# Kernel optimization log

Hardware: AMD Instinct MI355X
Metric: run time of the kernel (lower is better)

The kernel has to match this reference:

```python
import jax, jax.numpy as jnp
import numpy as np

ALPHA = 0.3        # Keras LeakyReLU default negative_slope
NUM_STEPS = 16     # fixed-step Dormand-Prince (see notes)
DEPTH = 10
HID = 1024
LOOK = 30
BATCH = 16384


def _leaky(x):
    return jnp.where(x > 0, x, ALPHA * x)


def _mlp(y, W1, b1, W2, b2, W3, b3):
    # drift f(y): 30 -> 1024 -> 1024 -> 30, autonomous (t unused)
    h = _leaky(jnp.dot(y, W1) + b1)
    h = _leaky(jnp.dot(h, W2) + b2)
    return jnp.dot(h, W3) + b3


def _dopri5_step(y, h, params):
    f = lambda z: _mlp(z, *params)
    k1 = f(y)
    k2 = f(y + h * (1.0 / 5.0) * k1)
    k3 = f(y + h * (3.0 / 40.0 * k1 + 9.0 / 40.0 * k2))
    k4 = f(y + h * (44.0 / 45.0 * k1 - 56.0 / 15.0 * k2 + 32.0 / 9.0 * k3))
    k5 = f(y + h * (19372.0 / 6561.0 * k1 - 25360.0 / 2187.0 * k2
                    + 64448.0 / 6561.0 * k3 - 212.0 / 729.0 * k4))
    k6 = f(y + h * (9017.0 / 3168.0 * k1 - 355.0 / 33.0 * k2
                    + 46732.0 / 5247.0 * k3 + 49.0 / 176.0 * k4
                    - 5103.0 / 18656.0 * k5))
    # 5th-order solution (b row of the Dormand-Prince tableau)
    return y + h * (35.0 / 384.0 * k1 + 500.0 / 1113.0 * k3
                    + 125.0 / 192.0 * k4 - 2187.0 / 6784.0 * k5
                    + 11.0 / 84.0 * k6)


def _solve_block(y0, params):
    # integrate dy/dt = f(y) from t=0 to t=1 with fixed step h
    h = 1.0 / NUM_STEPS
    def step(y, _):
        return _dopri5_step(y, h, params), None
    y, _ = jax.lax.scan(step, y0, None, length=NUM_STEPS)
    return y


def setup_inputs() -> dict:
    key = jax.random.key(0)
    ks = jax.random.split(key, 9)
    y0 = jax.random.normal(ks[0], (BATCH, 1, LOOK), dtype=jnp.float32)
    s1 = 1.0 / np.sqrt(LOOK)
    s2 = 1.0 / np.sqrt(HID)
    W1 = jax.random.normal(ks[1], (DEPTH, LOOK, HID), dtype=jnp.float32) * s1
    b1 = jnp.zeros((DEPTH, HID), dtype=jnp.float32)
    W2 = jax.random.normal(ks[2], (DEPTH, HID, HID), dtype=jnp.float32) * s2
    b2 = jnp.zeros((DEPTH, HID), dtype=jnp.float32)
    W3 = jax.random.normal(ks[3], (DEPTH, HID, LOOK), dtype=jnp.float32) * s2
    b3 = jnp.zeros((DEPTH, LOOK), dtype=jnp.float32)
    Wf = jax.random.normal(ks[4], (LOOK, 1), dtype=jnp.float32) * s1
    bf = jnp.zeros((1,), dtype=jnp.float32)
    return {"y0": y0, "W1": W1, "b1": b1, "W2": W2, "b2": b2,
            "W3": W3, "b3": b3, "Wf": Wf, "bf": bf}


def reference(y0, W1, b1, W2, b2, W3, b3, Wf, bf):
    # sequentially apply DEPTH ODE blocks, each with its own drift MLP
    def block(y, p):
        return _solve_block(y, p), None
    y, _ = jax.lax.scan(block, y0, (W1, b1, W2, b2, W3, b3))
    # final readout Dense(output_dim=1)
    return jnp.dot(y, Wf) + bf  # (B, 1, 1)
```

## Files before the change

### kernel.cpp

```cpp
#include <hip/hip_runtime.h>

#define BATCH 16384
#define LOOK 30
#define HID 1024
#define DEPTH 10
#define NSTEPS 16
#define ALPHA 0.3f

typedef short bf16x8 __attribute__((ext_vector_type(8)));
typedef float f32x4 __attribute__((ext_vector_type(4)));

__device__ __forceinline__ float leaky(float x) { return x > 0.f ? x : ALPHA * x; }

__device__ __forceinline__ unsigned short f2bf(float x) {
  unsigned u = __builtin_bit_cast(unsigned, x);
  unsigned r = u + 0x7FFFu + ((u >> 16) & 1u);
  return (unsigned short)(r >> 16);
}
__device__ __forceinline__ float bf2f(unsigned short b) {
  return __builtin_bit_cast(float, (unsigned)b << 16);
}

#define GLD_LDS16(g, l)                                        \
  __builtin_amdgcn_global_load_lds(                            \
      (const __attribute__((address_space(1))) void*)(g),      \
      (__attribute__((address_space(3))) void*)(l), 16, 0, 0)

__global__ __launch_bounds__(256) void k_w2split(const float* __restrict__ W2d,
                                                 short* __restrict__ W2Th,
                                                 short* __restrict__ W2Tl) {
  __shared__ float t[64][65];
  const int kb = blockIdx.x * 64;
  const int nb = blockIdx.y * 64;
  for (int i = threadIdx.x; i < 4096; i += 256) {
    int r = i >> 6, c = i & 63;
    t[r][c] = W2d[(size_t)(kb + r) * HID + nb + c];
  }
  __syncthreads();
  for (int i = threadIdx.x; i < 4096; i += 256) {
    int r = i >> 6, c = i & 63;
    float v = t[c][r];
    unsigned short hi = f2bf(v);
    unsigned short lo = f2bf(v - bf2f(hi));
    W2Th[(size_t)(nb + r) * HID + kb + c] = (short)hi;
    W2Tl[(size_t)(nb + r) * HID + kb + c] = (short)lo;
  }
}

__global__ __launch_bounds__(256) void k_w1t(const float* __restrict__ W1d,
                                             short* __restrict__ W1Th,
                                             short* __restrict__ W1Tl) {
  const int idx = blockIdx.x * 256 + threadIdx.x;
  if (idx >= 1024 * 32) return;
  const int n = idx >> 5, k = idx & 31;
  float v = (k < LOOK) ? W1d[(size_t)k * HID + n] : 0.f;
  unsigned short hi = f2bf(v);
  unsigned short lo = f2bf(v - bf2f(hi));
  W1Th[idx] = (short)hi;
  W1Tl[idx] = (short)lo;
}

__global__ __launch_bounds__(256) void k_w3t(const float* __restrict__ W3d,
                                             short* __restrict__ W3Th,
                                             short* __restrict__ W3Tl) {
  const int idx = blockIdx.x * 256 + threadIdx.x;
  if (idx >= 32 * 1024) return;
  const int n = idx >> 10, k = idx & 1023;
  float v = (n < LOOK) ? W3d[(size_t)k * LOOK + n] : 0.f;
  unsigned short hi = f2bf(v);
  unsigned short lo = f2bf(v - bf2f(hi));
  W3Th[idx] = (short)hi;
  W3Tl[idx] = (short)lo;
}

__global__ __launch_bounds__(256) void k_zinit(const float* __restrict__ y0,
                                               short* __restrict__ zh,
                                               short* __restrict__ zl) {
  const int idx = blockIdx.x * 256 + threadIdx.x;
  if (idx >= BATCH * 32) return;
  const int r = idx >> 5, c = idx & 31;
  float v = (c < LOOK) ? y0[(size_t)r * LOOK + c] : 0.f;
  unsigned short hi = f2bf(v);
  unsigned short lo = f2bf(v - bf2f(hi));
  zh[idx] = (short)hi;
  zl[idx] = (short)lo;
}

__global__ __launch_bounds__(512, 2) void k_l1(
    const short* __restrict__ zh, const short* __restrict__ zl,
    const short* __restrict__ W1Th, const short* __restrict__ W1Tl,
    const float* __restrict__ b1d, short* __restrict__ H1h,
    short* __restrict__ H1l) {
  __shared__ short za[2][128 * 32];
  const int tid = threadIdx.x, lane = tid & 63, wave = tid >> 6;
  const int row0 = blockIdx.x * 128;
  const int n0 = blockIdx.y * 256;
  const int wm = wave >> 2, wn = wave & 3;
  const int r15 = lane & 15;
  const int bk = (lane >> 4) * 8;

  bf16x8 bh[4], bl[4];
#pragma unroll
  for (int nj = 0; nj < 4; ++nj) {
    const size_t bo = (size_t)(n0 + wn * 64 + nj * 16 + r15) * 32 + bk;
    bh[nj] = *(const bf16x8*)&W1Th[bo];
    bl[nj] = *(const bf16x8*)&W1Tl[bo];
  }

  GLD_LDS16((const char*)(zh + (size_t)row0 * 32) + tid * 16, &za[0][tid * 8]);
  GLD_LDS16((const char*)(zl + (size_t)row0 * 32) + tid * 16, &za[1][tid * 8]);
  __syncthreads();

  bf16x8 ah[4], al[4];
#pragma unroll
  for (int mi = 0; mi < 4; ++mi) {
    const int ao = (wm * 64 + mi * 16 + r15) * 32 + bk;
    ah[mi] = *(const bf16x8*)&za[0][ao];
    al[mi] = *(const bf16x8*)&za[1][ao];
  }

  f32x4 acc[4][4];
#pragma unroll
  for (int i = 0; i < 4; ++i)
#pragma unroll
    for (int j = 0; j < 4; ++j) acc[i][j] = (f32x4){0.f, 0.f, 0.f, 0.f};

#pragma unroll
  for (int mi = 0; mi < 4; ++mi)
#pragma unroll
    for (int nj = 0; nj < 4; ++nj) {
      acc[mi][nj] = __builtin_amdgcn_mfma_f32_16x16x32_bf16(ah[mi], bh[nj],
                                                            acc[mi][nj], 0, 0, 0);
      acc[mi][nj] = __builtin_amdgcn_mfma_f32_16x16x32_bf16(ah[mi], bl[nj],
                                                            acc[mi][nj], 0, 0, 0);
      acc[mi][nj] = __builtin_amdgcn_mfma_f32_16x16x32_bf16(al[mi], bh[nj],
                                                            acc[mi][nj], 0, 0, 0);
    }

  const int crow = (lane >> 4) * 4;
#pragma unroll
  for (int nj = 0; nj < 4; ++nj) {
    const int col = n0 + wn * 64 + nj * 16 + r15;
    const float bias = b1d[col];
#pragma unroll
    for (int mi = 0; mi < 4; ++mi) {
      const int rb = row0 + wm * 64 + mi * 16 + crow;
#pragma unroll
      for (int r = 0; r < 4; ++r) {
        float v = leaky(acc[mi][nj][r] + bias);
        unsigned short hi = f2bf(v);
        unsigned short lo = f2bf(v - bf2f(hi));
        const size_t o = (size_t)(rb + r) * HID + col;
        H1h[o] = (short)hi;
        H1l[o] = (short)lo;
      }
    }
  }
}

__global__ __launch_bounds__(512, 2) void k_mid(
    const short* __restrict__ H1h, const short* __restrict__ H1l,
    const short* __restrict__ W2Th, const short* __restrict__ W2Tl,
    const float* __restrict__ b2d, short* __restrict__ H2h,
    short* __restrict__ H2l) {
  __shared__ char lds[131072];

  const int tid = threadIdx.x;
  const int lane = tid & 63;
  const int wave = tid >> 6;

  const int bid = blockIdx.x;
  const int wg = (bid & 7) * 32 + (bid >> 3);
  const int mb = wg >> 2, nb = wg & 3;
  const int row0 = mb * 256;
  const int n0 = nb * 256;
  const int wm = wave >> 2;
  const int wnb = wave & 3;

  const int l3 = lane >> 3;
  const int l7 = lane & 7;
  const int s = l7 ^ l3;
  const char* hsrc;
  const char* lsrc;
  int rbase;
  if (wave < 4) {
    hsrc = (const char*)H1h;
    lsrc = (const char*)H1l;
    rbase = row0;
  } else {
    hsrc = (const char*)W2Th;
    lsrc = (const char*)W2Tl;
    rbase = n0;
  }
  const char* srcB[8];
#pragma unroll
  for (int i = 0; i < 8; ++i) {
    const int c = wave * 8 + i;
    const int rloc = (c & 31) * 8 + l3;
    const char* base = (s < 4) ? hsrc : lsrc;
    srcB[i] = base + (size_t)(rbase + rloc) * 2048 + (size_t)(s & 3) * 16;
  }
  const int dchunk0 = wave * 8 * 1024;

  int offA0, offA1, offB0, offB1;
  {
    const int r15 = lane & 15;
    const int kq = lane >> 4;
    const int pa0 = ((0 * 4 + kq) ^ l7) * 16;
    const int pa1 = ((1 * 4 + kq) ^ l7) * 16;
    offA0 = (wm * 128 + r15) * 128 + pa0;
    offA1 = (wm * 128 + r15) * 128 + pa1;
    offB0 = 32768 + (wnb * 64 + r15) * 128 + pa0;
    offB1 = 32768 + (wnb * 64 + r15) * 128 + pa1;
  }

  f32x4 acc[8][4];
#pragma unroll
  for (int i = 0; i < 8; ++i)
#pragma unroll
    for (int j = 0; j < 4; ++j) acc[i][j] = (f32x4){0.f, 0.f, 0.f, 0.f};

#define STAGE(buf, kb)                                                   \
  {                                                                      \
    _Pragma("unroll") for (int i = 0; i < 8; ++i) {                      \
      GLD_LDS16(srcB[i] + (kb), &lds[(buf)*65536 + dchunk0 + i * 1024]); \
    }                                                                    \
  }

  STAGE(0, 0);
  __syncthreads();

  int cur = 0;
  for (int t = 0; t < 32; ++t) {
    if (t < 31) STAGE(cur ^ 1, (t + 1) * 64);

    const char* buf = &lds[cur * 65536];
    bf16x8 bh[4], bl[4];
#pragma unroll
    for (int nj = 0; nj < 4; ++nj) {
      bh[nj] = *(const bf16x8*)(buf + offB0 + nj * 2048);
      bl[nj] = *(const bf16x8*)(buf + offB1 + nj * 2048);
    }
#pragma unroll
    for (int mi = 0; mi < 8; ++mi) {
      bf16x8 ah = *(const bf16x8*)(buf + offA0 + mi * 2048);
      bf16x8 al = *(const bf16x8*)(buf + offA1 + mi * 2048);
#pragma unroll
      for (int nj = 0; nj < 4; ++nj) {
        acc[mi][nj] =
            __builtin_amdgcn_mfma_f32_16x16x32_bf16(ah, bh[nj], acc[mi][nj], 0, 0, 0);
        acc[mi][nj] =
            __builtin_amdgcn_mfma_f32_16x16x32_bf16(ah, bl[nj], acc[mi][nj], 0, 0, 0);
        acc[mi][nj] =
            __builtin_amdgcn_mfma_f32_16x16x32_bf16(al, bh[nj], acc[mi][nj], 0, 0, 0);
      }
    }
    __syncthreads();
    cur ^= 1;
  }
#undef STAGE

  const int crow = (lane >> 4) * 4;
  const int ccol = lane & 15;
#pragma unroll
  for (int nj = 0; nj < 4; ++nj) {
    const int col = n0 + wnb * 64 + nj * 16 + ccol;
    const float bv = b2d[col];
#pragma unroll
    for (int mi = 0; mi < 8; ++mi) {
      const int rb = row0 + wm * 128 + mi * 16 + crow;
#pragma unroll
      for (int r = 0; r < 4; ++r) {
        float v = leaky(acc[mi][nj][r] + bv);
        unsigned short hi = f2bf(v);
        unsigned short lo = f2bf(v - bf2f(hi));
        const size_t o = (size_t)(rb + r) * HID + col;
        H2h[o] = (short)hi;
        H2l[o] = (short)lo;
      }
    }
  }
}

__global__ __launch_bounds__(256, 4) void k_l3(
    const short* __restrict__ H2h, const short* __restrict__ H2l,
    const short* __restrict__ W3Th, const short* __restrict__ W3Tl,
    const float* __restrict__ b3d, float* __restrict__ kout,
    const float* __restrict__ K0, const float* __restrict__ K1,
    const float* __restrict__ K2, const float* __restrict__ K3,
    const float* __restrict__ K4, float* __restrict__ y,
    short* __restrict__ zh, short* __restrict__ zl, int combine, float p1,
    float p2, float p3, float p4, float p5, float pc, float hb1, float hb2,
    float hb3, float hb4, float hb5, float hb6) {
  __shared__ short lds[2][4096];

  const int tid = threadIdx.x, lane = tid & 63, wave = tid >> 6;
  const int row0 = blockIdx.x * 32;
  const int wm = wave & 1, wn = wave >> 1;

  const int half = tid >> 7;
  const int idx = tid & 127;
  const int srow = idx >> 2;
  const int sd = idx & 3;
  const int slog = sd ^ ((srow >> 1) & 3);
  const short* Asrc = half ? H2l : H2h;
  const short* Bsrc = half ? W3Tl : W3Th;
  const char* aSrc = (const char*)(Asrc + (size_t)(row0 + srow) * HID) + slog * 16;
  const char* bSrc = (const char*)(Bsrc + (size_t)srow * HID) + slog * 16;
  short* aDst0 = &lds[0][half * 1024 + idx * 8];
  short* bDst0 = &lds[0][2048 + half * 1024 + idx * 8];
  short* aDst1 = &lds[1][half * 1024 + idx * 8];
  short* bDst1 = &lds[1][2048 + half * 1024 + idx * 8];

  const int r15 = lane & 15;
  const int kc = lane >> 4;
  const int aRow = wm * 16 + r15;
  const int bRow = wn * 16 + r15;
  const int aOff = aRow * 32 + (kc ^ ((aRow >> 1) & 3)) * 8;
  const int bOff = 2048 + bRow * 32 + (kc ^ ((bRow >> 1) & 3)) * 8;

  f32x4 acc = (f32x4){0.f, 0.f, 0.f, 0.f};

#define STAGE3(ad, bd, kb)          \
  {                                 \
    GLD_LDS16(aSrc + (kb), (ad));   \
    GLD_LDS16(bSrc + (kb), (bd));   \
  }

  STAGE3(aDst0, bDst0, 0);
  __syncthreads();

  for (int t = 0; t < 32; ++t) {
    const int cur = t & 1;
    if (t < 31) {
      if (cur == 0) STAGE3(aDst1, bDst1, (t + 1) * 64)
      else STAGE3(aDst0, bDst0, (t + 1) * 64)
    }
    const short* buf = lds[cur];
    bf16x8 ah = *(const bf16x8*)(buf + aOff);
    bf16x8 al = *(const bf16x8*)(buf + 1024 + aOff);
    bf16x8 bh = *(const bf16x8*)(buf + bOff);
    bf16x8 bl = *(const bf16x8*)(buf + 1024 + bOff);
    acc = __builtin_amdgcn_mfma_f32_16x16x32_bf16(ah, bh, acc, 0, 0, 0);
    acc = __builtin_amdgcn_mfma_f32_16x16x32_bf16(ah, bl, acc, 0, 0, 0);
    acc = __builtin_amdgcn_mfma_f32_16x16x32_bf16(al, bh, acc, 0, 0, 0);
    __syncthreads();
  }
#undef STAGE3

  const int c = wn * 16 + r15;
  const int rb = row0 + wm * 16 + (lane >> 4) * 4;
  const float bias = (c < LOOK) ? b3d[c] : 0.f;
#pragma unroll
  for (int r = 0; r < 4; ++r) {
    const int row = rb + r;
    const float kv = acc[r] + bias;
    float zv = 0.f;
    if (c < LOOK) {
      const size_t id = (size_t)row * LOOK + c;
      const float yv = y[id];
      if (combine) {
        float yn = yv + hb1 * K0[id] + hb2 * K1[id] + hb3 * K2[id] +
                   hb4 * K3[id] + hb5 * K4[id] + hb6 * kv;
        y[id] = yn;
        zv = yn;
      } else {
        kout[id] = kv;
        zv = yv + pc * kv;
        if (p1 != 0.f) zv += p1 * K0[id];
        if (p2 != 0.f) zv += p2 * K1[id];
        if (p3 != 0.f) zv += p3 * K2[id];
        if (p4 != 0.f) zv += p4 * K3[id];
        if (p5 != 0.f) zv += p5 * K4[id];
      }
    }
    unsigned short hi = f2bf(zv);
    unsigned short lo = f2bf(zv - bf2f(hi));
    const size_t zo = (size_t)row * 32 + c;
    zh[zo] = (short)hi;
    zl[zo] = (short)lo;
  }
}

__global__ __launch_bounds__(256) void k_readout(const float* __restrict__ y,
                                                 const float* __restrict__ Wf,
                                                 const float* __restrict__ bf,
                                                 float* __restrict__ out) {
  const int r = blockIdx.x * blockDim.x + threadIdx.x;
  if (r >= BATCH) return;
  float acc = bf[0];
#pragma unroll
  for (int c = 0; c < LOOK; ++c) acc += y[(size_t)r * LOOK + c] * Wf[c];
  out[r] = acc;
}

extern "C" void kernel_launch(void* const* d_in, const int* in_sizes, int n_in,
                              void* d_out, int out_size, void* d_ws,
                              size_t ws_size, hipStream_t stream) {
  const float* y0 = (const float*)d_in[0];
  const float* W1 = (const float*)d_in[1];
  const float* b1 = (const float*)d_in[2];
  const float* W2 = (const float*)d_in[3];
  const float* b2 = (const float*)d_in[4];
  const float* W3 = (const float*)d_in[5];
  const float* b3 = (const float*)d_in[6];
  const float* Wf = (const float*)d_in[7];
  const float* bf = (const float*)d_in[8];
  float* out = (float*)d_out;

  const size_t NY = (size_t)BATCH * LOOK;
  float* f = (float*)d_ws;
  float* y = f;
  float* kk[5];
  for (int i = 0; i < 5; ++i) kk[i] = f + NY * (1 + i);
  char* p = (char*)(f + NY * 6);
  short* zh = (short*)p; p += (size_t)BATCH * 32 * 2;
  short* zl = (short*)p; p += (size_t)BATCH * 32 * 2;
  short* H1h = (short*)p; p += (size_t)BATCH * HID * 2;
  short* H1l = (short*)p; p += (size_t)BATCH * HID * 2;
  short* H2h = (short*)p; p += (size_t)BATCH * HID * 2;
  short* H2l = (short*)p; p += (size_t)BATCH * HID * 2;
  short* W2Th = (short*)p; p += (size_t)HID * HID * 2;
  short* W2Tl = (short*)p; p += (size_t)HID * HID * 2;
  short* W1Th = (short*)p; p += (size_t)HID * 32 * 2;
  short* W1Tl = (short*)p; p += (size_t)HID * 32 * 2;
  short* W3Th = (short*)p; p += (size_t)32 * HID * 2;
  short* W3Tl = (short*)p;

  hipMemcpyAsync(y, y0, NY * sizeof(float), hipMemcpyDeviceToDevice, stream);
  k_zinit<<<dim3(BATCH * 32 / 256), 256, 0, stream>>>(y0, zh, zl);

  const double hh = 1.0 / 16.0;
  static const double A[6][5] = {
      {0, 0, 0, 0, 0},
      {1.0 / 5, 0, 0, 0, 0},
      {3.0 / 40, 9.0 / 40, 0, 0, 0},
      {44.0 / 45, -56.0 / 15, 32.0 / 9, 0, 0},
      {19372.0 / 6561, -25360.0 / 2187, 64448.0 / 6561, -212.0 / 729, 0},
      {9017.0 / 3168, -355.0 / 33, 46732.0 / 5247, 49.0 / 176,
       -5103.0 / 18656},
  };
  static const double Bb[6] = {35.0 / 384,  0,              500.0 / 1113,
                               125.0 / 192, -2187.0 / 6784, 11.0 / 84};

  const float hb1 = (float)(hh * Bb[0]);
  const float hb2 = (float)(hh * Bb[1]);
  const float hb3 = (float)(hh * Bb[2]);
  const float hb4 = (float)(hh * Bb[3]);
  const float hb5 = (float)(hh * Bb[4]);
  const float hb6 = (float)(hh * Bb[5]);

  for (int d = 0; d < DEPTH; ++d) {
    const float* W1d = W1 + (size_t)d * LOOK * HID;
    const float* b1d = b1 + (size_t)d * HID;
    const float* W2d = W2 + (size_t)d * HID * HID;
    const float* b2d = b2 + (size_t)d * HID;
    const float* W3d = W3 + (size_t)d * HID * LOOK;
    const float* b3d = b3 + (size_t)d * LOOK;

    k_w2split<<<dim3(16, 16), 256, 0, stream>>>(W2d, W2Th, W2Tl);
    k_w1t<<<dim3(128), 256, 0, stream>>>(W1d, W1Th, W1Tl);
    k_w3t<<<dim3(128), 256, 0, stream>>>(W3d, W3Th, W3Tl);

    for (int s = 0; s < NSTEPS; ++s) {
      for (int st = 0; st < 6; ++st) {
        float pv[5] = {0.f, 0.f, 0.f, 0.f, 0.f};
        float pc = 0.f;
        if (st < 5) {
          for (int jj = 0; jj < 5; ++jj)
            if (jj < st) pv[jj] = (float)(hh * A[st + 1][jj]);
          pc = (float)(hh * A[st + 1][st]);
        }
        k_l1<<<dim3(BATCH / 128, HID / 256), 512, 0, stream>>>(
            zh, zl, W1Th, W1Tl, b1d, H1h, H1l);
        k_mid<<<dim3(256), 512, 0, stream>>>(H1h, H1l, W2Th, W2Tl, b2d, H2h,
                                             H2l);
        const int comb = (st == 5) ? 1 : 0;
        float* kout = (st < 5) ? kk[st] : kk[0];
        k_l3<<<dim3(BATCH / 32), 256, 0, stream>>>(
            H2h, H2l, W3Th, W3Tl, b3d, kout, kk[0], kk[1], kk[2], kk[3],
            kk[4], y, zh, zl, comb, pv[0], pv[1], pv[2], pv[3], pv[4], pc,
            hb1, hb2, hb3, hb4, hb5, hb6);
      }
    }
  }

  k_readout<<<dim3(BATCH / 256), 256, 0, stream>>>(y, Wf, bf, out);
}
```

Measured before the change: 137.6 ms.

## Fuse layer-1 GEMM into layer-3 epilogue and pretranspose all W1 once

Folds the 30->1024 first-layer matmul into the tail of the layer-3 kernel. Each block stages the new stage input z in shared memory and computes H1 directly with MFMA, which removes the separate k_l1 launch and the z round-trip through global memory. All depths of W1 are split and transposed once up front, so the next block's W1 can be selected at the final stage of each depth. The fused kernel drops occupancy to 2 blocks per CU and writes the full H1 tensor from fewer, smaller blocks, which may cost bandwidth efficiency.

Measured after the change: 130.7 ms. -5.0%, faster.

```diff
diff --git a/kernel.cpp b/kernel.cpp
--- a/kernel.cpp
+++ b/kernel.cpp
@@ -47,13 +47,15 @@
   }
 }
 
-__global__ __launch_bounds__(256) void k_w1t(const float* __restrict__ W1d,
-                                             short* __restrict__ W1Th,
-                                             short* __restrict__ W1Tl) {
+__global__ __launch_bounds__(256) void k_w1t_all(const float* __restrict__ W1,
+                                                 short* __restrict__ W1Th,
+                                                 short* __restrict__ W1Tl) {
   const int idx = blockIdx.x * 256 + threadIdx.x;
-  if (idx >= 1024 * 32) return;
-  const int n = idx >> 5, k = idx & 31;
-  float v = (k < LOOK) ? W1d[(size_t)k * HID + n] : 0.f;
+  if (idx >= DEPTH * 1024 * 32) return;
+  const int d = idx >> 15;
+  const int rem = idx & 32767;
+  const int n = rem >> 5, k = rem & 31;
+  float v = (k < LOOK) ? W1[(size_t)d * LOOK * HID + (size_t)k * HID + n] : 0.f;
   unsigned short hi = f2bf(v);
   unsigned short lo = f2bf(v - bf2f(hi));
   W1Th[idx] = (short)hi;
@@ -176,43 +178,40 @@
   const int n0 = nb * 256;
   const int wm = wave >> 2;
   const int wnb = wave & 3;
-
+  const int r15 = lane & 15;
+  const int kq = lane >> 4;
+  const int l7 = lane & 7;
   const int l3 = lane >> 3;
-  const int l7 = lane & 7;
-  const int s = l7 ^ l3;
-  const char* hsrc;
-  const char* lsrc;
-  int rbase;
-  if (wave < 4) {
-    hsrc = (const char*)H1h;
-    lsrc = (const char*)H1l;
-    rbase = row0;
-  } else {
-    hsrc = (const char*)W2Th;
-    lsrc = (const char*)W2Tl;
-    rbase = n0;
-  }
+
   const char* srcB[8];
-#pragma unroll
-  for (int i = 0; i < 8; ++i) {
-    const int c = wave * 8 + i;
-    const int rloc = (c & 31) * 8 + l3;
+  {
+    const int s = l7 ^ l3;
+    const char* hsrc;
+    const char* lsrc;
+    int rbase;
+    if (wave < 4) {
+      hsrc = (const char*)H1h;
+      lsrc = (const char*)H1l;
+      rbase = row0;
+    } else {
+      hsrc = (const char*)W2Th;
+      lsrc = (const char*)W2Tl;
+      rbase = n0;
+    }
     const char* base = (s < 4) ? hsrc : lsrc;
-    srcB[i] = base + (size_t)(rbase + rloc) * 2048 + (size_t)(s & 3) * 16;
-  }
-  const int dchunk0 = wave * 8 * 1024;
-
-  int offA0, offA1, offB0, offB1;
-  {
-    const int r15 = lane & 15;
-    const int kq = lane >> 4;
-    const int pa0 = ((0 * 4 + kq) ^ l7) * 16;
-    const int pa1 = ((1 * 4 + kq) ^ l7) * 16;
-    offA0 = (wm * 128 + r15) * 128 + pa0;
-    offA1 = (wm * 128 + r15) * 128 + pa1;
-    offB0 = 32768 + (wnb * 64 + r15) * 128 + pa0;
-    offB1 = 32768 + (wnb * 64 + r15) * 128 + pa1;
-  }
+#pragma unroll
+    for (int i = 0; i < 8; ++i) {
+      const int c = wave * 8 + i;
+      const int rloc = (c & 31) * 8 + l3;
+      srcB[i] = base + (size_t)(rbase + rloc) * 2048 + (size_t)(s & 3) * 16;
+    }
+  }
+  const int dchunk0 = wave * 8192;
+
+  const int offA0 = (wm * 128 + r15) * 128 + ((0 + kq) ^ l7) * 16;
+  const int offA1 = (wm * 128 + r15) * 128 + ((4 + kq) ^ l7) * 16;
+  const int offB0 = 32768 + (wnb * 64 + r15) * 128 + ((0 + kq) ^ l7) * 16;
+  const int offB1 = 32768 + (wnb * 64 + r15) * 128 + ((4 + kq) ^ l7) * 16;
 
   f32x4 acc[8][4];
 #pragma unroll
@@ -261,10 +260,9 @@
 #undef STAGE
 
   const int crow = (lane >> 4) * 4;
-  const int ccol = lane & 15;
 #pragma unroll
   for (int nj = 0; nj < 4; ++nj) {
-    const int col = n0 + wnb * 64 + nj * 16 + ccol;
+    const int col = n0 + wnb * 64 + nj * 16 + r15;
     const float bv = b2d[col];
 #pragma unroll
     for (int mi = 0; mi < 8; ++mi) {
@@ -282,17 +280,20 @@
   }
 }
 
-__global__ __launch_bounds__(256, 4) void k_l3(
+__global__ __launch_bounds__(256, 2) void k_l3l1(
     const short* __restrict__ H2h, const short* __restrict__ H2l,
     const short* __restrict__ W3Th, const short* __restrict__ W3Tl,
     const float* __restrict__ b3d, float* __restrict__ kout,
     const float* __restrict__ K0, const float* __restrict__ K1,
     const float* __restrict__ K2, const float* __restrict__ K3,
-    const float* __restrict__ K4, float* __restrict__ y,
-    short* __restrict__ zh, short* __restrict__ zl, int combine, float p1,
-    float p2, float p3, float p4, float p5, float pc, float hb1, float hb2,
-    float hb3, float hb4, float hb5, float hb6) {
+    const float* __restrict__ K4, float* __restrict__ y, int combine,
+    float p1, float p2, float p3, float p4, float p5, float pc, float hb1,
+    float hb2, float hb3, float hb4, float hb5, float hb6,
+    const short* __restrict__ W1Tnh, const short* __restrict__ W1Tnl,
+    const float* __restrict__ b1n, short* __restrict__ H1h,
+    short* __restrict__ H1l) {
   __shared__ short lds[2][4096];
+  __shared__ short zs[2][32][40];
 
   const int tid = threadIdx.x, lane = tid & 63, wave = tid >> 6;
   const int row0 = blockIdx.x * 32;
@@ -348,37 +349,78 @@
   }
 #undef STAGE3
 
-  const int c = wn * 16 + r15;
-  const int rb = row0 + wm * 16 + (lane >> 4) * 4;
-  const float bias = (c < LOOK) ? b3d[c] : 0.f;
-#pragma unroll
-  for (int r = 0; r < 4; ++r) {
-    const int row = rb + r;
-    const float kv = acc[r] + bias;
-    float zv = 0.f;
-    if (c < LOOK) {
-      const size_t id = (size_t)row * LOOK + c;
-      const float yv = y[id];
-      if (combine) {
-        float yn = yv + hb1 * K0[id] + hb2 * K1[id] + hb3 * K2[id] +
-                   hb4 * K3[id] + hb5 * K4[id] + hb6 * kv;
-        y[id] = yn;
-        zv = yn;
-      } else {
-        kout[id] = kv;
-        zv = yv + pc * kv;
-        if (p1 != 0.f) zv += p1 * K0[id];
-        if (p2 != 0.f) zv += p2 * K1[id];
-        if (p3 != 0.f) zv += p3 * K2[id];
-        if (p4 != 0.f) zv += p4 * K3[id];
-        if (p5 != 0.f) zv += p5 * K4[id];
+  {
+    const int c = wn * 16 + r15;
+    const int rb = wm * 16 + (lane >> 4) * 4;
+    const float bias = (c < LOOK) ? b3d[c] : 0.f;
+#pragma unroll
+    for (int r = 0; r < 4; ++r) {
+      const int rloc = rb + r;
+      const int row = row0 + rloc;
+      const float kv = acc[r] + bias;
+      float zv = 0.f;
+      if (c < LOOK) {
+        const size_t id = (size_t)row * LOOK + c;
+        const float yv = y[id];
+        if (combine) {
+          float yn = yv + hb1 * K0[id] + hb2 * K1[id] + hb3 * K2[id] +
+                     hb4 * K3[id] + hb5 * K4[id] + hb6 * kv;
+          y[id] = yn;
+          zv = yn;
+        } else {
+          kout[id] = kv;
+          zv = yv + pc * kv;
+          if (p1 != 0.f) zv += p1 * K0[id];
+          if (p2 != 0.f) zv += p2 * K1[id];
+          if (p3 != 0.f) zv += p3 * K2[id];
+          if (p4 != 0.f) zv += p4 * K3[id];
+          if (p5 != 0.f) zv += p5 * K4[id];
+        }
       }
-    }
-    unsigned short hi = f2bf(zv);
-    unsigned short lo = f2bf(zv - bf2f(hi));
-    const size_t zo = (size_t)row * 32 + c;
-    zh[zo] = (short)hi;
-    zl[zo] = (short)lo;
+      unsigned short hi = f2bf(zv);
+      unsigned short lo = f2bf(zv - bf2f(hi));
+      zs[0][rloc][c] = (short)hi;
+      zs[1][rloc][c] = (short)lo;
+    }
+  }
+  __syncthreads();
+
+  bf16x8 zfh[2], zfl[2];
+#pragma unroll
+  for (int mi = 0; mi < 2; ++mi) {
+    zfh[mi] = *(const bf16x8*)&zs[0][mi * 16 + r15][kc * 8];
+    zfl[mi] = *(const bf16x8*)&zs[1][mi * 16 + r15][kc * 8];
+  }
+  const int crow = (lane >> 4) * 4;
+#pragma unroll
+  for (int nj = 0; nj < 16; ++nj) {
+    const int col = wave * 256 + nj * 16 + r15;
+    const size_t bo = (size_t)col * 32 + kc * 8;
+    bf16x8 bh = *(const bf16x8*)&W1Tnh[bo];
+    bf16x8 bl = *(const bf16x8*)&W1Tnl[bo];
+    f32x4 a0 = (f32x4){0.f, 0.f, 0.f, 0.f};
+    f32x4 a1 = (f32x4){0.f, 0.f, 0.f, 0.f};
+    a0 = __builtin_amdgcn_mfma_f32_16x16x32_bf16(zfh[0], bh, a0, 0, 0, 0);
+    a0 = __builtin_amdgcn_mfma_f32_16x16x32_bf16(zfh[0], bl, a0, 0, 0, 0);
+    a0 = __builtin_amdgcn_mfma_f32_16x16x32_bf16(zfl[0], bh, a0, 0, 0, 0);
+    a1 = __builtin_amdgcn_mfma_f32_16x16x32_bf16(zfh[1], bh, a1, 0, 0, 0);
+    a1 = __builtin_amdgcn_mfma_f32_16x16x32_bf16(zfh[1], bl, a1, 0, 0, 0);
+    a1 = __builtin_amdgcn_mfma_f32_16x16x32_bf16(zfl[1], bh, a1, 0, 0, 0);
+    const float bias = b1n[col];
+#pragma unroll
+    for (int mi = 0; mi < 2; ++mi) {
+      const f32x4 av = mi ? a1 : a0;
+      const int rbase = row0 + mi * 16 + crow;
+#pragma unroll
+      for (int r = 0; r < 4; ++r) {
+        float v = leaky(av[r] + bias);
+        unsigned short hi = f2bf(v);
+        unsigned short lo = f2bf(v - bf2f(hi));
+        const size_t o = (size_t)(rbase + r) * HID + col;
+        H1h[o] = (short)hi;
+        H1l[o] = (short)lo;
+      }
+    }
   }
 }
 
@@ -422,13 +464,17 @@
   short* H2l = (short*)p; p += (size_t)BATCH * HID * 2;
   short* W2Th = (short*)p; p += (size_t)HID * HID * 2;
   short* W2Tl = (short*)p; p += (size_t)HID * HID * 2;
-  short* W1Th = (short*)p; p += (size_t)HID * 32 * 2;
-  short* W1Tl = (short*)p; p += (size_t)HID * 32 * 2;
+  short* W1Th = (short*)p; p += (size_t)DEPTH * HID * 32 * 2;
+  short* W1Tl = (short*)p; p += (size_t)DEPTH * HID * 32 * 2;
   short* W3Th = (short*)p; p += (size_t)32 * HID * 2;
   short* W3Tl = (short*)p;
 
   hipMemcpyAsync(y, y0, NY * sizeof(float), hipMemcpyDeviceToDevice, stream);
+
+  k_w1t_all<<<dim3(DEPTH * 1024 * 32 / 256), 256, 0, stream>>>(W1, W1Th, W1Tl);
   k_zinit<<<dim3(BATCH * 32 / 256), 256, 0, stream>>>(y0, zh, zl);
+  k_l1<<<dim3(BATCH / 128, HID / 256), 512, 0, stream>>>(zh, zl, W1Th, W1Tl,
+                                                         b1, H1h, H1l);
 
   const double hh = 1.0 / 16.0;
   static const double A[6][5] = {
@@ -451,15 +497,12 @@
   const float hb6 = (float)(hh * Bb[5]);
 
   for (int d = 0; d < DEPTH; ++d) {
-    const float* W1d = W1 + (size_t)d * LOOK * HID;
-    const float* b1d = b1 + (size_t)d * HID;
     const float* W2d = W2 + (size_t)d * HID * HID;
     const float* b2d = b2 + (size_t)d * HID;
     const float* W3d = W3 + (size_t)d * HID * LOOK;
     const float* b3d = b3 + (size_t)d * LOOK;
 
     k_w2split<<<dim3(16, 16), 256, 0, stream>>>(W2d, W2Th, W2Tl);
-    k_w1t<<<dim3(128), 256, 0, stream>>>(W1d, W1Th, W1Tl);
     k_w3t<<<dim3(128), 256, 0, stream>>>(W3d, W3Th, W3Tl);
 
     for (int s = 0; s < NSTEPS; ++s) {
@@ -471,16 +514,20 @@
             if (jj < st) pv[jj] = (float)(hh * A[st + 1][jj]);
           pc = (float)(hh * A[st + 1][st]);
         }
-        k_l1<<<dim3(BATCH / 128, HID / 256), 512, 0, stream>>>(
-            zh, zl, W1Th, W1Tl, b1d, H1h, H1l);
+        int dn = d;
+        if (st == 5 && s == NSTEPS - 1) dn = (d + 1 < DEPTH) ? d + 1 : d;
+        const short* W1Tnh = W1Th + (size_t)dn * HID * 32;
+        const short* W1Tnl = W1Tl + (size_t)dn * HID * 32;
+        const float* b1n = b1 + (size_t)dn * HID;
+
         k_mid<<<dim3(256), 512, 0, stream>>>(H1h, H1l, W2Th, W2Tl, b2d, H2h,
                                              H2l);
         const int comb = (st == 5) ? 1 : 0;
         float* kout = (st < 5) ? kk[st] : kk[0];
-        k_l3<<<dim3(BATCH / 32), 256, 0, stream>>>(
+        k_l3l1<<<dim3(BATCH / 32), 256, 0, stream>>>(
             H2h, H2l, W3Th, W3Tl, b3d, kout, kk[0], kk[1], kk[2], kk[3],
-            kk[4], y, zh, zl, comb, pv[0], pv[1], pv[2], pv[3], pv[4], pc,
-            hb1, hb2, hb3, hb4, hb5, hb6);
+            kk[4], y, comb, pv[0], pv[1], pv[2], pv[3], pv[4], pc, hb1, hb2,
+            hb3, hb4, hb5, hb6, W1Tnh, W1Tnl, b1n, H1h, H1l);
       }
     }
   }
```
